# Performance work log

Hardware: AMD Instinct MI355X
Metric: run time of the kernel (lower is better)

The kernel has to match this reference:

```python
import jax, jax.numpy as jnp
import numpy as np

DIM = 768
MID = 256
HEADS = 12
P_SCALE = 0.8
SCALE = (DIM // HEADS) ** -0.5


def setup_inputs() -> dict:
    key = jax.random.key(0)
    ks = jax.random.split(key, 9)
    B, N, C = 64, 197, DIM
    s = 0.02
    return {
        "x": jax.random.normal(ks[0], (B, N, C), jnp.float32),
        "qkv_w": jax.random.normal(ks[1], (3 * C, C), jnp.float32) * s,
        "qkv_b": jax.random.normal(ks[2], (3 * C,), jnp.float32) * s,
        "proj_w": jax.random.normal(ks[3], (C, C), jnp.float32) * s,
        "proj_b": jax.random.normal(ks[4], (C,), jnp.float32) * s,
        "down_w": jax.random.normal(ks[5], (MID, C), jnp.float32) * s,
        "down_b": jax.random.normal(ks[6], (MID,), jnp.float32) * s,
        "up_w": jax.random.normal(ks[7], (2 * C, MID), jnp.float32) * s,
        "up_b": jax.random.normal(ks[8], (2 * C,), jnp.float32) * s,
    }


def reference(x, qkv_w, qkv_b, proj_w, proj_b, down_w, down_b, up_w, up_b):
    B, N, C = x.shape
    H, D = HEADS, C // HEADS
    # Adapter: down -> tanh -> up gives kv prefix; q prefix is zeros
    kv_prefix = jnp.tanh(x @ down_w.T + down_b) @ up_w.T + up_b  # [B,N,2C]
    prefix = jnp.concatenate([jnp.zeros((B, N, C), x.dtype), kv_prefix], -1)
    qkv = (x @ qkv_w.T + qkv_b) + P_SCALE * prefix  # [B,N,3C]
    qkv = qkv.reshape(B, N, 3, H, D).transpose(2, 0, 3, 1, 4)  # [3,B,H,N,D]
    q, k, v = qkv[0], qkv[1], qkv[2]
    attn = jax.nn.softmax(jnp.einsum("bhnd,bhmd->bhnm", q, k) * SCALE, axis=-1)
    out = jnp.einsum("bhnm,bhmd->bhnd", attn, v)  # [B,H,N,D]
    out = out.transpose(0, 2, 1, 3).reshape(B, N, C)
    return out @ proj_w.T + proj_b
```

## Files before the change

### kernel.cpp

```cpp
#include <hip/hip_runtime.h>
#include <hip/hip_bf16.h>
#include <stdint.h>

#define DIM   768
#define MID   256
#define HEADS 12
#define NB    64
#define NN    197
#define NT    (NB*NN)
#define QKVC  2304
#define NCOMB 2560

typedef __attribute__((ext_vector_type(4))) float f32x4;
typedef __attribute__((ext_vector_type(8))) short s8v;

__device__ __forceinline__ unsigned short f2b(float f) {
    union { float f; unsigned int u; } x; x.f = f;
    unsigned int u = x.u;
    unsigned int r = (u + 0x7FFFu + ((u >> 16) & 1u)) >> 16;
    return (unsigned short)r;
}
__device__ __forceinline__ float b2f(unsigned short s) {
    union { unsigned int u; float f; } x; x.u = ((unsigned int)s) << 16;
    return x.f;
}

__device__ __forceinline__ void gld_lds16(const void* g, void* l) {
    __builtin_amdgcn_global_load_lds(
        (const __attribute__((address_space(1))) unsigned int*)g,
        (__attribute__((address_space(3))) unsigned int*)l, 16, 0, 0);
}

__global__ void cast_all(const float* __restrict__ x,
                         const float* __restrict__ qkv_w,
                         const float* __restrict__ down_w,
                         const float* __restrict__ up_w,
                         const float* __restrict__ proj_w,
                         unsigned short* __restrict__ xb,
                         unsigned short* __restrict__ o_comb,
                         unsigned short* __restrict__ o_up,
                         unsigned short* __restrict__ o_proj) {
    int blk = blockIdx.x;
    if (blk < 2048) {
        const int n4 = NT * DIM / 4;
        for (int i = blk * 256 + threadIdx.x; i < n4; i += 2048 * 256) {
            float4 v = ((const float4*)x)[i];
            ushort4 o;
            o.x = f2b(v.x); o.y = f2b(v.y); o.z = f2b(v.z); o.w = f2b(v.w);
            ((ushort4*)xb)[i] = o;
        }
        return;
    }
    blk -= 2048;
    const float* in; unsigned short* out; int base;
    if (blk < 1728)      { in = qkv_w;  out = o_comb;              base = blk; }
    else if (blk < 1920) { in = down_w; out = o_comb + QKVC * DIM; base = blk - 1728; }
    else if (blk < 2304) { in = up_w;   out = o_up;                base = blk - 1920; }
    else                 { in = proj_w; out = o_proj;              base = blk - 2304; }
    int i = base * 256 + threadIdx.x;
    float4 v = ((const float4*)in)[i];
    ushort4 o;
    o.x = f2b(v.x); o.y = f2b(v.y); o.z = f2b(v.z); o.w = f2b(v.w);
    ((ushort4*)out)[i] = o;
}

template<int EPI>
__global__ __launch_bounds__(256) void gemm_bt(
    const unsigned short* __restrict__ A,
    const unsigned short* __restrict__ W,
    const float* __restrict__ bias0,
    const float* __restrict__ bias1,
    int M, int K, int GN,
    unsigned short* __restrict__ ob0,
    unsigned short* __restrict__ ob1,
    float* __restrict__ outf)
{
    __shared__ __align__(16) unsigned short lds[3][2][128 * 32];
    const int tid = threadIdx.x;
    const int l = tid & 63;
    const int w = tid >> 6;
    const int wr = w >> 1, wc = w & 1;

    const int nwg = gridDim.x;
    const int orig = blockIdx.x;
    const int q8 = nwg >> 3, r8 = nwg & 7;
    const int xcd = orig & 7, slice = orig >> 3;
    const int wgid = (xcd < r8 ? xcd * (q8 + 1)
                               : r8 * (q8 + 1) + (xcd - r8) * q8) + slice;
    const int bm = wgid / GN;
    const int bn = wgid - bm * GN;

    f32x4 acc[4][4];
#pragma unroll
    for (int m = 0; m < 4; ++m)
#pragma unroll
        for (int n = 0; n < 4; ++n)
            acc[m][n] = (f32x4){0.f, 0.f, 0.f, 0.f};

    const int KT = K >> 5;

    const int src = (((tid & 3) ^ ((tid >> 3) & 3)) << 3);
    const int dst = ((tid & 3) << 3);
    const int dA0 = (tid >> 2) * 32 + dst;
    const int dA1 = dA0 + 64 * 32;
    int ra0 = bm * 128 + (tid >> 2);      if (ra0 > M - 1) ra0 = M - 1;
    int ra1 = bm * 128 + 64 + (tid >> 2); if (ra1 > M - 1) ra1 = M - 1;
    const int rb0 = bn * 128 + (tid >> 2);
    const int rb1 = rb0 + 64;
    const unsigned short* pa0 = A + (size_t)ra0 * K + src;
    const unsigned short* pa1 = A + (size_t)ra1 * K + src;
    const unsigned short* pb0 = W + (size_t)rb0 * K + src;
    const unsigned short* pb1 = W + (size_t)rb1 * K + src;

    auto stage = [&](int buf) {
        gld_lds16(pa0, &lds[buf][0][dA0]);
        gld_lds16(pb0, &lds[buf][1][dA0]);
        gld_lds16(pa1, &lds[buf][0][dA1]);
        gld_lds16(pb1, &lds[buf][1][dA1]);
        pa0 += 32; pa1 += 32; pb0 += 32; pb1 += 32;
    };

    stage(0);
    stage(1);

    const int rsl = (((l >> 4) ^ ((l >> 1) & 3)) << 3);
    int cb = 0;
    int sb = 2;
    for (int kt = 0; kt < KT; ++kt) {
        if (kt + 1 < KT) asm volatile("s_waitcnt vmcnt(4)" ::: "memory");
        else             asm volatile("s_waitcnt vmcnt(0)" ::: "memory");
        __builtin_amdgcn_s_barrier();
        asm volatile("" ::: "memory");
        if (kt + 2 < KT) stage(sb);
        const unsigned short* la = lds[cb][0];
        const unsigned short* lb = lds[cb][1];
        s8v a[4], b[4];
#pragma unroll
        for (int m = 0; m < 4; ++m)
            a[m] = *(const s8v*)&la[(wr * 64 + m * 16 + (l & 15)) * 32 + rsl];
#pragma unroll
        for (int n = 0; n < 4; ++n)
            b[n] = *(const s8v*)&lb[(wc * 64 + n * 16 + (l & 15)) * 32 + rsl];
        __builtin_amdgcn_s_setprio(1);
#pragma unroll
        for (int m = 0; m < 4; ++m)
#pragma unroll
            for (int n = 0; n < 4; ++n)
                acc[m][n] = __builtin_amdgcn_mfma_f32_16x16x32_bf16(a[m], b[n], acc[m][n], 0, 0, 0);
        __builtin_amdgcn_s_setprio(0);
        cb = (cb == 2) ? 0 : cb + 1;
        sb = (sb == 2) ? 0 : sb + 1;
    }
    __syncthreads();

    if (EPI == 0) {
        unsigned short* stg = ((unsigned short*)lds) + w * (16 * 68);
        const int C0 = bn * 128 + wc * 64;
        const bool ish = (C0 >= QKVC);
#pragma unroll
        for (int mq = 0; mq < 4; ++mq) {
#pragma unroll
            for (int n = 0; n < 4; ++n) {
                int c = C0 + n * 16 + (l & 15);
                float bi = ish ? bias1[c - QKVC] : bias0[c];
                float sc2 = (c < DIM) ? 0.125f : 1.0f;
#pragma unroll
                for (int j = 0; j < 4; ++j) {
                    float v = acc[mq][n][j] + bi;
                    v = ish ? tanhf(v) : v * sc2;
                    stg[((l >> 4) * 4 + j) * 68 + n * 16 + (l & 15)] = f2b(v);
                }
            }
#pragma unroll
            for (int p = 0; p < 2; ++p) {
                int rr2 = p * 8 + (l >> 3);
                int r = bm * 128 + wr * 64 + mq * 16 + rr2;
                s8v v = *(const s8v*)&stg[rr2 * 68 + (l & 7) * 8];
                if (r < M) {
                    if (!ish) *(s8v*)&ob0[(size_t)r * QKVC + C0 + (l & 7) * 8] = v;
                    else      *(s8v*)&ob1[(size_t)r * MID + (C0 - QKVC) + (l & 7) * 8] = v;
                }
            }
        }
    } else if (EPI == 1) {
        unsigned short* stg = ((unsigned short*)lds) + w * (16 * 68);
        const int C0 = bn * 128 + wc * 64;
#pragma unroll
        for (int mq = 0; mq < 4; ++mq) {
#pragma unroll
            for (int n = 0; n < 4; ++n) {
                int c = C0 + n * 16 + (l & 15);
                float bi = bias0[c];
#pragma unroll
                for (int j = 0; j < 4; ++j)
                    stg[((l >> 4) * 4 + j) * 68 + n * 16 + (l & 15)] =
                        f2b(0.8f * (acc[mq][n][j] + bi));
            }
#pragma unroll
            for (int p = 0; p < 2; ++p) {
                int rr2 = p * 8 + (l >> 3);
                int r = bm * 128 + wr * 64 + mq * 16 + rr2;
                if (r < M) {
                    size_t base = (size_t)r * QKVC + DIM + C0 + (l & 7) * 8;
                    s8v add = *(const s8v*)&stg[rr2 * 68 + (l & 7) * 8];
                    s8v old = *(const s8v*)&ob0[base];
                    s8v res;
#pragma unroll
                    for (int i = 0; i < 8; ++i)
                        res[i] = (short)f2b(b2f((unsigned short)old[i]) +
                                            b2f((unsigned short)add[i]));
                    *(s8v*)&ob0[base] = res;
                }
            }
        }
    } else {
#pragma unroll
        for (int n = 0; n < 4; ++n) {
            int c = bn * 128 + wc * 64 + n * 16 + (l & 15);
            float bi = bias0[c];
#pragma unroll
            for (int m = 0; m < 4; ++m) {
#pragma unroll
                for (int j = 0; j < 4; ++j) {
                    int r = bm * 128 + wr * 64 + m * 16 + (l >> 4) * 4 + j;
                    if (r >= M) continue;
                    outf[(size_t)r * DIM + c] = acc[m][n][j] + bi;
                }
            }
        }
    }
}

#define NKV  224
#define VPAD 232
#define PSP  40

__global__ __launch_bounds__(256) void attn_kernel(
    const unsigned short* __restrict__ qkv,
    unsigned short* __restrict__ ob)
{
    __shared__ __align__(16) unsigned short Ks[NKV * 64];
    __shared__ __align__(16) unsigned short Vt[64 * VPAD];
    __shared__ __align__(16) unsigned short Ps[4][16][PSP];

    const int tid = threadIdx.x;
    const int l = tid & 63;
    const int w = tid >> 6;
    const int bh = blockIdx.x;
    const int b = bh / HEADS, h = bh - b * HEADS;
    const unsigned short* qp = qkv + (size_t)(b * NN) * QKVC + h * 64;
    const unsigned short* kp = qp + DIM;
    const unsigned short* vp = qp + 2 * DIM;

    const s8v zer = (s8v){0, 0, 0, 0, 0, 0, 0, 0};

    for (int e = tid; e < NKV * 8; e += 256) {
        int r = e >> 3, ch = e & 7;
        int idx = (r * 64 + ch * 8) ^ ((r & 7) << 3);
        s8v val = (r < NN) ? *(const s8v*)&kp[(size_t)r * QKVC + ch * 8] : zer;
        *(s8v*)&Ks[idx] = val;
    }
    for (int e = tid; e < NKV * 8; e += 256) {
        int r = e >> 3, ch = e & 7;
        s8v val = (r < NN) ? *(const s8v*)&vp[(size_t)r * QKVC + ch * 8] : zer;
#pragma unroll
        for (int i = 0; i < 8; ++i)
            Vt[(ch * 8 + i) * VPAD + r] = (unsigned short)val[i];
    }
    __syncthreads();

    unsigned short* psw = &Ps[w][0][0];

    for (int qc = 0; qc < 4; ++qc) {
        const int rbase = qc * 64 + w * 16;
        s8v aq[2];
#pragma unroll
        for (int kc = 0; kc < 2; ++kc) {
            int r = rbase + (l & 15); if (r > NN - 1) r = NN - 1;
            aq[kc] = *(const s8v*)&qp[(size_t)r * QKVC + kc * 32 + (l >> 4) * 8];
        }
        f32x4 sacc[14];
#pragma unroll
        for (int t = 0; t < 14; ++t) sacc[t] = (f32x4){0.f, 0.f, 0.f, 0.f};
#pragma unroll
        for (int t = 0; t < 14; ++t) {
            int col = t * 16 + (l & 15);
#pragma unroll
            for (int kc = 0; kc < 2; ++kc) {
                int idx = (col * 64 + kc * 32 + (l >> 4) * 8) ^ ((col & 7) << 3);
                s8v bk = *(const s8v*)&Ks[idx];
                sacc[t] = __builtin_amdgcn_mfma_f32_16x16x32_bf16(aq[kc], bk, sacc[t], 0, 0, 0);
            }
        }
        float mx[4] = {-1e30f, -1e30f, -1e30f, -1e30f};
#pragma unroll
        for (int t = 0; t < 14; ++t) {
            int col = t * 16 + (l & 15);
            if (col < NN) {
#pragma unroll
                for (int j = 0; j < 4; ++j) mx[j] = fmaxf(mx[j], sacc[t][j]);
            }
        }
#pragma unroll
        for (int j = 0; j < 4; ++j)
#pragma unroll
            for (int off = 1; off < 16; off <<= 1)
                mx[j] = fmaxf(mx[j], __shfl_xor(mx[j], off, 64));

        float sm[4] = {0.f, 0.f, 0.f, 0.f};
        f32x4 oacc[4];
#pragma unroll
        for (int n = 0; n < 4; ++n) oacc[n] = (f32x4){0.f, 0.f, 0.f, 0.f};
#pragma unroll
        for (int kc = 0; kc < 7; ++kc) {
#pragma unroll
            for (int th = 0; th < 2; ++th) {
                const int t = kc * 2 + th;
                int col = t * 16 + (l & 15);
#pragma unroll
                for (int j = 0; j < 4; ++j) {
                    float p = (col < NN) ? __expf(sacc[t][j] - mx[j]) : 0.f;
                    sm[j] += p;
                    psw[((l >> 4) * 4 + j) * PSP + th * 16 + (l & 15)] = f2b(p);
                }
            }
            s8v ap = *(const s8v*)&psw[(l & 15) * PSP + (l >> 4) * 8];
#pragma unroll
            for (int n = 0; n < 4; ++n) {
                s8v bv = *(const s8v*)&Vt[(n * 16 + (l & 15)) * VPAD + kc * 32 + (l >> 4) * 8];
                oacc[n] = __builtin_amdgcn_mfma_f32_16x16x32_bf16(ap, bv, oacc[n], 0, 0, 0);
            }
        }
#pragma unroll
        for (int j = 0; j < 4; ++j)
#pragma unroll
            for (int off = 1; off < 16; off <<= 1)
                sm[j] += __shfl_xor(sm[j], off, 64);

#pragma unroll
        for (int n = 0; n < 4; ++n) {
#pragma unroll
            for (int j = 0; j < 4; ++j) {
                int r = rbase + (l >> 4) * 4 + j;
                if (r < NN) {
                    float val = oacc[n][j] / sm[j];
                    ob[((size_t)(b * NN + r)) * DIM + h * 64 + n * 16 + (l & 15)] = f2b(val);
                }
            }
        }
    }
}

extern "C" void kernel_launch(void* const* d_in, const int* in_sizes, int n_in,
                              void* d_out, int out_size, void* d_ws, size_t ws_size,
                              hipStream_t stream) {
    const float* x      = (const float*)d_in[0];
    const float* qkv_w  = (const float*)d_in[1];
    const float* qkv_b  = (const float*)d_in[2];
    const float* proj_w = (const float*)d_in[3];
    const float* proj_b = (const float*)d_in[4];
    const float* down_w = (const float*)d_in[5];
    const float* down_b = (const float*)d_in[6];
    const float* up_w   = (const float*)d_in[7];
    const float* up_b   = (const float*)d_in[8];
    float* out = (float*)d_out;

    char* ws = (char*)d_ws;
    size_t off = 0;
    unsigned short* xb      = (unsigned short*)(ws + off); off += (size_t)NT * DIM * 2;
    unsigned short* wcomb   = (unsigned short*)(ws + off); off += (size_t)NCOMB * DIM * 2;
    unsigned short* up_wb   = (unsigned short*)(ws + off); off += (size_t)2 * DIM * MID * 2;
    unsigned short* proj_wb = (unsigned short*)(ws + off); off += (size_t)DIM * DIM * 2;
    unsigned short* hbuf    = (unsigned short*)(ws + off); off += (size_t)NT * MID * 2;
    unsigned short* qkvbuf  = (unsigned short*)(ws + off); off += (size_t)NT * QKVC * 2;
    unsigned short* obuf    = xb;

    cast_all<<<2048 + 2880, 256, 0, stream>>>(x, qkv_w, down_w, up_w, proj_w,
                                              xb, wcomb, up_wb, proj_wb);

    const int GM1 = (NT + 127) / 128;
    gemm_bt<0><<<GM1 * (NCOMB / 128), 256, 0, stream>>>(xb, wcomb, qkv_b, down_b,
                                                        NT, DIM, NCOMB / 128,
                                                        qkvbuf, hbuf, nullptr);
    gemm_bt<1><<<GM1 * (2 * DIM / 128), 256, 0, stream>>>(hbuf, up_wb, up_b, nullptr,
                                                          NT, MID, 2 * DIM / 128,
                                                          qkvbuf, nullptr, nullptr);
    attn_kernel<<<NB * HEADS, 256, 0, stream>>>(qkvbuf, obuf);
    gemm_bt<2><<<GM1 * (DIM / 128), 256, 0, stream>>>(obuf, proj_wb, proj_b, nullptr,
                                                      NT, DIM, DIM / 128,
                                                      nullptr, nullptr, out);
}
```

Baseline: 190.0 us.

## Replace 4-wave 128x128 GEMM with single-wave 64x64 tiles, double-buffered

Swaps the 256-thread, 128x128-tile, triple-buffered GEMM for a 64-thread, one-wave 64x64 tile kernel with double buffering, so no barriers are needed. NT=12608 divides exactly by 64, so the M-bounds checks are dropped. Each wave still computes a 64x64 block, but now loads its whole A and B tile alone instead of sharing through LDS, which doubles global/LDS traffic per FLOP. It also loses the deeper prefetch pipeline and relies on many more small workgroups for latency hiding.

```diff
diff --git a/kernel.cpp b/kernel.cpp
--- a/kernel.cpp
+++ b/kernel.cpp
@@ -65,7 +65,7 @@
 }
 
 template<int EPI>
-__global__ __launch_bounds__(256) void gemm_bt(
+__global__ __launch_bounds__(64) void gemm_wp(
     const unsigned short* __restrict__ A,
     const unsigned short* __restrict__ W,
     const float* __restrict__ bias0,
@@ -75,11 +75,8 @@
     unsigned short* __restrict__ ob1,
     float* __restrict__ outf)
 {
-    __shared__ __align__(16) unsigned short lds[3][2][128 * 32];
-    const int tid = threadIdx.x;
-    const int l = tid & 63;
-    const int w = tid >> 6;
-    const int wr = w >> 1, wc = w & 1;
+    __shared__ __align__(16) unsigned short lds[2][2][64 * 32];
+    const int l = threadIdx.x;
 
     const int nwg = gridDim.x;
     const int orig = blockIdx.x;
@@ -99,48 +96,41 @@
 
     const int KT = K >> 5;
 
-    const int src = (((tid & 3) ^ ((tid >> 3) & 3)) << 3);
-    const int dst = ((tid & 3) << 3);
-    const int dA0 = (tid >> 2) * 32 + dst;
-    const int dA1 = dA0 + 64 * 32;
-    int ra0 = bm * 128 + (tid >> 2);      if (ra0 > M - 1) ra0 = M - 1;
-    int ra1 = bm * 128 + 64 + (tid >> 2); if (ra1 > M - 1) ra1 = M - 1;
-    const int rb0 = bn * 128 + (tid >> 2);
-    const int rb1 = rb0 + 64;
-    const unsigned short* pa0 = A + (size_t)ra0 * K + src;
-    const unsigned short* pa1 = A + (size_t)ra1 * K + src;
-    const unsigned short* pb0 = W + (size_t)rb0 * K + src;
-    const unsigned short* pb1 = W + (size_t)rb1 * K + src;
+    const int src = (((l & 3) ^ ((l >> 3) & 3)) << 3);
+    const int dst = (l >> 2) * 32 + (l & 3) * 8;
+    const unsigned short* pa = A + (size_t)(bm * 64 + (l >> 2)) * K + src;
+    const unsigned short* pb = W + (size_t)(bn * 64 + (l >> 2)) * K + src;
+    const size_t rstep = (size_t)16 * K;
 
     auto stage = [&](int buf) {
-        gld_lds16(pa0, &lds[buf][0][dA0]);
-        gld_lds16(pb0, &lds[buf][1][dA0]);
-        gld_lds16(pa1, &lds[buf][0][dA1]);
-        gld_lds16(pb1, &lds[buf][1][dA1]);
-        pa0 += 32; pa1 += 32; pb0 += 32; pb1 += 32;
+#pragma unroll
+        for (int p = 0; p < 4; ++p) {
+            gld_lds16(pa + p * rstep, &lds[buf][0][dst + p * 16 * 32]);
+            gld_lds16(pb + p * rstep, &lds[buf][1][dst + p * 16 * 32]);
+        }
+        pa += 32; pb += 32;
     };
 
     stage(0);
-    stage(1);
 
     const int rsl = (((l >> 4) ^ ((l >> 1) & 3)) << 3);
-    int cb = 0;
-    int sb = 2;
+    int buf = 0;
     for (int kt = 0; kt < KT; ++kt) {
-        if (kt + 1 < KT) asm volatile("s_waitcnt vmcnt(4)" ::: "memory");
-        else             asm volatile("s_waitcnt vmcnt(0)" ::: "memory");
-        __builtin_amdgcn_s_barrier();
-        asm volatile("" ::: "memory");
-        if (kt + 2 < KT) stage(sb);
-        const unsigned short* la = lds[cb][0];
-        const unsigned short* lb = lds[cb][1];
+        if (kt + 1 < KT) {
+            stage(buf ^ 1);
+            asm volatile("s_waitcnt vmcnt(8)" ::: "memory");
+        } else {
+            asm volatile("s_waitcnt vmcnt(0)" ::: "memory");
+        }
+        const unsigned short* la = lds[buf][0];
+        const unsigned short* lb = lds[buf][1];
         s8v a[4], b[4];
 #pragma unroll
         for (int m = 0; m < 4; ++m)
-            a[m] = *(const s8v*)&la[(wr * 64 + m * 16 + (l & 15)) * 32 + rsl];
+            a[m] = *(const s8v*)&la[(m * 16 + (l & 15)) * 32 + rsl];
 #pragma unroll
         for (int n = 0; n < 4; ++n)
-            b[n] = *(const s8v*)&lb[(wc * 64 + n * 16 + (l & 15)) * 32 + rsl];
+            b[n] = *(const s8v*)&lb[(n * 16 + (l & 15)) * 32 + rsl];
         __builtin_amdgcn_s_setprio(1);
 #pragma unroll
         for (int m = 0; m < 4; ++m)
@@ -148,14 +138,13 @@
             for (int n = 0; n < 4; ++n)
                 acc[m][n] = __builtin_amdgcn_mfma_f32_16x16x32_bf16(a[m], b[n], acc[m][n], 0, 0, 0);
         __builtin_amdgcn_s_setprio(0);
-        cb = (cb == 2) ? 0 : cb + 1;
-        sb = (sb == 2) ? 0 : sb + 1;
-    }
-    __syncthreads();
+        buf ^= 1;
+    }
+
+    unsigned short* stg = (unsigned short*)lds;
+    const int C0 = bn * 64;
 
     if (EPI == 0) {
-        unsigned short* stg = ((unsigned short*)lds) + w * (16 * 68);
-        const int C0 = bn * 128 + wc * 64;
         const bool ish = (C0 >= QKVC);
 #pragma unroll
         for (int mq = 0; mq < 4; ++mq) {
@@ -172,19 +161,15 @@
                 }
             }
 #pragma unroll
-            for (int p = 0; p < 2; ++p) {
-                int rr2 = p * 8 + (l >> 3);
-                int r = bm * 128 + wr * 64 + mq * 16 + rr2;
+            for (int p2 = 0; p2 < 2; ++p2) {
+                int rr2 = p2 * 8 + (l >> 3);
+                int r = bm * 64 + mq * 16 + rr2;
                 s8v v = *(const s8v*)&stg[rr2 * 68 + (l & 7) * 8];
-                if (r < M) {
-                    if (!ish) *(s8v*)&ob0[(size_t)r * QKVC + C0 + (l & 7) * 8] = v;
-                    else      *(s8v*)&ob1[(size_t)r * MID + (C0 - QKVC) + (l & 7) * 8] = v;
-                }
+                if (!ish) *(s8v*)&ob0[(size_t)r * QKVC + C0 + (l & 7) * 8] = v;
+                else      *(s8v*)&ob1[(size_t)r * MID + (C0 - QKVC) + (l & 7) * 8] = v;
             }
         }
     } else if (EPI == 1) {
-        unsigned short* stg = ((unsigned short*)lds) + w * (16 * 68);
-        const int C0 = bn * 128 + wc * 64;
 #pragma unroll
         for (int mq = 0; mq < 4; ++mq) {
 #pragma unroll
@@ -197,33 +182,30 @@
                         f2b(0.8f * (acc[mq][n][j] + bi));
             }
 #pragma unroll
-            for (int p = 0; p < 2; ++p) {
-                int rr2 = p * 8 + (l >> 3);
-                int r = bm * 128 + wr * 64 + mq * 16 + rr2;
-                if (r < M) {
-                    size_t base = (size_t)r * QKVC + DIM + C0 + (l & 7) * 8;
-                    s8v add = *(const s8v*)&stg[rr2 * 68 + (l & 7) * 8];
-                    s8v old = *(const s8v*)&ob0[base];
-                    s8v res;
-#pragma unroll
-                    for (int i = 0; i < 8; ++i)
-                        res[i] = (short)f2b(b2f((unsigned short)old[i]) +
-                                            b2f((unsigned short)add[i]));
-                    *(s8v*)&ob0[base] = res;
-                }
+            for (int p2 = 0; p2 < 2; ++p2) {
+                int rr2 = p2 * 8 + (l >> 3);
+                int r = bm * 64 + mq * 16 + rr2;
+                size_t base = (size_t)r * QKVC + DIM + C0 + (l & 7) * 8;
+                s8v add = *(const s8v*)&stg[rr2 * 68 + (l & 7) * 8];
+                s8v old = *(const s8v*)&ob0[base];
+                s8v res;
+#pragma unroll
+                for (int i = 0; i < 8; ++i)
+                    res[i] = (short)f2b(b2f((unsigned short)old[i]) +
+                                        b2f((unsigned short)add[i]));
+                *(s8v*)&ob0[base] = res;
             }
         }
     } else {
 #pragma unroll
         for (int n = 0; n < 4; ++n) {
-            int c = bn * 128 + wc * 64 + n * 16 + (l & 15);
+            int c = C0 + n * 16 + (l & 15);
             float bi = bias0[c];
 #pragma unroll
             for (int m = 0; m < 4; ++m) {
 #pragma unroll
                 for (int j = 0; j < 4; ++j) {
-                    int r = bm * 128 + wr * 64 + m * 16 + (l >> 4) * 4 + j;
-                    if (r >= M) continue;
+                    int r = bm * 64 + m * 16 + (l >> 4) * 4 + j;
                     outf[(size_t)r * DIM + c] = acc[m][n][j] + bi;
                 }
             }
@@ -378,15 +360,15 @@
     cast_all<<<2048 + 2880, 256, 0, stream>>>(x, qkv_w, down_w, up_w, proj_w,
                                               xb, wcomb, up_wb, proj_wb);
 
-    const int GM1 = (NT + 127) / 128;
-    gemm_bt<0><<<GM1 * (NCOMB / 128), 256, 0, stream>>>(xb, wcomb, qkv_b, down_b,
-                                                        NT, DIM, NCOMB / 128,
-                                                        qkvbuf, hbuf, nullptr);
-    gemm_bt<1><<<GM1 * (2 * DIM / 128), 256, 0, stream>>>(hbuf, up_wb, up_b, nullptr,
-                                                          NT, MID, 2 * DIM / 128,
-                                                          qkvbuf, nullptr, nullptr);
+    const int GM = NT / 64;
+    gemm_wp<0><<<GM * (NCOMB / 64), 64, 0, stream>>>(xb, wcomb, qkv_b, down_b,
+                                                     NT, DIM, NCOMB / 64,
+                                                     qkvbuf, hbuf, nullptr);
+    gemm_wp<1><<<GM * (2 * DIM / 64), 64, 0, stream>>>(hbuf, up_wb, up_b, nullptr,
+                                                       NT, MID, 2 * DIM / 64,
+                                                       qkvbuf, nullptr, nullptr);
     attn_kernel<<<NB * HEADS, 256, 0, stream>>>(qkvbuf, obuf);
-    gemm_bt<2><<<GM1 * (DIM / 128), 256, 0, stream>>>(obuf, proj_wb, proj_b, nullptr,
-                                                      NT, DIM, DIM / 128,
-                                                      nullptr, nullptr, out);
-}
+    gemm_wp<2><<<GM * (DIM / 64), 64, 0, stream>>>(obuf, proj_wb, proj_b, nullptr,
+                                                   NT, DIM, DIM / 64,
+                                                   nullptr, nullptr, out);
+}
```

Result: slower. 242.5 us (+27.6%).
